# Optimization experiments

Measured on AMD Instinct MI355X. Metric: run time of the kernel, lower is better.

## Reference

```python
import jax, jax.numpy as jnp
import numpy as np

N_EMBD = 1024
N_HEAD = 16
HEAD_DIM = N_EMBD // N_HEAD


def setup_inputs() -> dict:
    key = jax.random.key(0)
    ks = jax.random.split(key, 9)
    B, T, C = 2, 2048, N_EMBD
    s = 1.0 / np.sqrt(C)
    inp = {
        "x": jax.random.normal(ks[0], (B, T, C), dtype=jnp.float32),
        "Wq": jax.random.normal(ks[1], (C, C), dtype=jnp.float32) * s,
        "bq": jnp.zeros((C,), dtype=jnp.float32),
        "Wk": jax.random.normal(ks[2], (C, C), dtype=jnp.float32) * s,
        "bk": jnp.zeros((C,), dtype=jnp.float32),
        "Wv": jax.random.normal(ks[3], (C, C), dtype=jnp.float32) * s,
        "bv": jnp.zeros((C,), dtype=jnp.float32),
        "Wo": jax.random.normal(ks[4], (C, C), dtype=jnp.float32) * s,
        "bo": jnp.zeros((C,), dtype=jnp.float32),
    }
    return inp


def reference(x, Wq, bq, Wk, bk, Wv, bv, Wo, bo):
    B, T, C = x.shape
    H, D = N_HEAD, HEAD_DIM
    # projections (torch Linear: x @ W^T + b)
    q = (x @ Wq.T + bq).reshape(B, T, H, D).transpose(0, 2, 1, 3)  # [B,H,T,D]
    k = (x @ Wk.T + bk).reshape(B, T, H, D).transpose(0, 2, 1, 3)
    v = (x @ Wv.T + bv).reshape(B, T, H, D).transpose(0, 2, 1, 3)
    scores = jnp.einsum("bhqd,bhkd->bhqk", q, k) / jnp.sqrt(jnp.asarray(D, x.dtype))
    causal = jnp.tril(jnp.ones((T, T), dtype=bool))
    scores = jnp.where(causal[None, None], scores, jnp.asarray(-jnp.inf, x.dtype))
    weights = jax.nn.softmax(scores, axis=-1)  # [B,H,T,T]
    attended = jnp.einsum("bhqk,bhkd->bhqd", weights, v)
    attended = attended.transpose(0, 2, 1, 3).reshape(B, T, C)
    return attended @ Wo.T + bo
```

## Files before the change

kernel.cpp:

```cpp
#include <hip/hip_runtime.h>

typedef unsigned short u16;
typedef __attribute__((ext_vector_type(8))) __bf16 bf16x8;
typedef __attribute__((ext_vector_type(4))) float f32x4;
typedef __attribute__((ext_vector_type(4))) unsigned int u32x4;

#define MFMA16(a, b, c) __builtin_amdgcn_mfma_f32_16x16x32_bf16(a, b, c, 0, 0, 0)

__device__ __forceinline__ u16 f2bf(float f) {
    unsigned u = __float_as_uint(f);
    u = (u + 0x7FFFu + ((u >> 16) & 1u)) >> 16;
    return (u16)u;
}

__device__ __forceinline__ void gl_lds16(const u16* g, u16* l) {
    __builtin_amdgcn_global_load_lds(
        (const __attribute__((address_space(1))) unsigned int*)g,
        (__attribute__((address_space(3))) unsigned int*)l, 16, 0, 0);
}

static constexpr int Bv = 2, Tv = 2048, Cv = 1024, Hv = 16, Dv = 64;
static constexpr int Mv = Bv * Tv;

static constexpr size_t OFF_XB = 0;
static constexpr size_t OFF_WQ = 4194304;
static constexpr size_t OFF_WK = OFF_WQ + 1048576;
static constexpr size_t OFF_WV = OFF_WK + 1048576;
static constexpr size_t OFF_WO = OFF_WV + 1048576;
static constexpr size_t OFF_Q  = OFF_WO + 1048576;
static constexpr size_t OFF_K  = OFF_Q + 4194304;
static constexpr size_t OFF_VT = OFF_K + 4194304;
static constexpr size_t OFF_A  = OFF_VT + 4194304;

__global__ __launch_bounds__(256) void convert_all(
    const float* __restrict__ x,
    const float* __restrict__ wq, const float* __restrict__ wk,
    const float* __restrict__ wv, const float* __restrict__ wo,
    u16* __restrict__ dst)
{
    int i4 = blockIdx.x * blockDim.x + threadIdx.x;
    if (i4 >= 2097152) return;
    int idx = i4 * 4;
    const float* src; int off;
    if (idx < 4194304) { src = x; off = idx; }
    else {
        int rel = idx - 4194304;
        int j = rel >> 20;
        off = rel & 1048575;
        src = (j == 0) ? wq : (j == 1) ? wk : (j == 2) ? wv : wo;
    }
    float4 v = *(const float4*)(src + off);
    ushort4 o;
    o.x = f2bf(v.x); o.y = f2bf(v.y); o.z = f2bf(v.z); o.w = f2bf(v.w);
    *(ushort4*)(dst + idx) = o;
}

template <bool OUT_BF16, bool ROWBIAS>
__device__ __forceinline__ void gemm128_b32(
    u16* __restrict__ lA0, u16* __restrict__ lB0,
    u16* __restrict__ lA1, u16* __restrict__ lB1,
    const u16* __restrict__ A, const u16* __restrict__ Wt,
    const float* __restrict__ bias, void* __restrict__ outp,
    int m0, int n0, int N, int K)
{
    const int tid  = threadIdx.x;
    const int lane = tid & 63, w = tid >> 6;
    const int quad = lane >> 4, lm = lane & 15;
    const int wm = (w & 1) * 64, wn = (w >> 1) * 64;
    const int h4A = (w & 1) * 4, h4B = ((w >> 1) & 1) * 4;
    const int rowi = lane >> 3, seg = lane & 7;
    const int raw = seg ^ rowi;
    const int hh  = raw >> 2, qq = raw & 3;

    f32x4 zero = {0.f, 0.f, 0.f, 0.f};
    f32x4 acc[4][4];
    #pragma unroll
    for (int mt = 0; mt < 4; mt++)
        #pragma unroll
        for (int nt = 0; nt < 4; nt++) acc[mt][nt] = zero;

    auto stage = [&](u16* dA, u16* dB, int k0) __attribute__((always_inline)) {
        #pragma unroll
        for (int j = 0; j < 2; j++) {
            int pr0 = w * 16 + j * 8;
            int gr  = pr0 + rowi + (hh << 6);
            gl_lds16(A  + (size_t)(m0 + gr) * K + k0 + qq * 8, &dA[pr0 * 64]);
            gl_lds16(Wt + (size_t)(n0 + gr) * K + k0 + qq * 8, &dB[pr0 * 64]);
        }
    };
    auto compute = [&](const u16* sA, const u16* sB) __attribute__((always_inline)) {
        bf16x8 af[4], bf[4];
        #pragma unroll
        for (int mt = 0; mt < 4; mt++)
            af[mt] = *(const bf16x8*)&sA[(mt * 16 + lm) * 64 + (((h4A + quad) ^ (lm & 7)) * 8)];
        #pragma unroll
        for (int nt = 0; nt < 4; nt++)
            bf[nt] = *(const bf16x8*)&sB[(nt * 16 + lm) * 64 + (((h4B + quad) ^ (lm & 7)) * 8)];
        #pragma unroll
        for (int mt = 0; mt < 4; mt++)
            #pragma unroll
            for (int nt = 0; nt < 4; nt++)
                acc[mt][nt] = MFMA16(af[mt], bf[nt], acc[mt][nt]);
    };

    const int NT = K >> 5;
    stage(lA0, lB0, 0);
    stage(lA1, lB1, 32);
    for (int t = 0; t < NT; ++t) {
        if (t + 1 < NT) asm volatile("s_waitcnt vmcnt(4)" ::: "memory");
        else            asm volatile("s_waitcnt vmcnt(0)" ::: "memory");
        __builtin_amdgcn_s_barrier();
        const u16* sA = (t & 1) ? lA1 : lA0;
        const u16* sB = (t & 1) ? lB1 : lB0;
        compute(sA, sB);
        asm volatile("s_waitcnt lgkmcnt(0)" ::: "memory");
        __builtin_amdgcn_s_barrier();
        if (t + 2 < NT) stage((t & 1) ? lA1 : lA0, (t & 1) ? lB1 : lB0, (t + 2) << 5);
    }

    #pragma unroll
    for (int nt = 0; nt < 4; nt++) {
        int col = n0 + wn + nt * 16 + lm;
        float cb = ROWBIAS ? 0.f : bias[col];
        #pragma unroll
        for (int mt = 0; mt < 4; mt++) {
            #pragma unroll
            for (int r = 0; r < 4; r++) {
                int row = m0 + wm + mt * 16 + quad * 4 + r;
                float v = acc[mt][nt][r] + (ROWBIAS ? bias[row] : cb);
                if (OUT_BF16) ((u16*)outp)[(size_t)row * N + col] = f2bf(v);
                else          ((float*)outp)[(size_t)row * N + col] = v;
            }
        }
    }
}

__global__ __launch_bounds__(256, 3) void gemm_qkv(
    const u16* __restrict__ A,
    const u16* __restrict__ Wq, const u16* __restrict__ Wk, const u16* __restrict__ Wv,
    const float* __restrict__ bq, const float* __restrict__ bk, const float* __restrict__ bv,
    u16* __restrict__ Q, u16* __restrict__ K, u16* __restrict__ VT)
{
    __shared__ u16 lA0[64 * 64];
    __shared__ u16 lB0[64 * 64];
    __shared__ u16 lA1[64 * 64];
    __shared__ u16 lB1[64 * 64];

    int bid = blockIdx.x;
    int sw  = (bid & 7) * 96 + (bid >> 3);
    int g2  = sw >> 5;
    int row = sw & 31;
    int which = g2 >> 3, col = g2 & 7;

    if (which == 0) {
        gemm128_b32<true, false>(lA0, lB0, lA1, lB1, A, Wq, bq, Q, row * 128, col * 128, Cv, Cv);
    } else if (which == 1) {
        gemm128_b32<true, false>(lA0, lB0, lA1, lB1, A, Wk, bk, K, row * 128, col * 128, Cv, Cv);
    } else {
        gemm128_b32<true, true>(lA0, lB0, lA1, lB1, Wv, A, bv, VT, col * 128, row * 128, Mv, Cv);
    }
}

__global__ __launch_bounds__(512) void gemm_o64(
    const u16* __restrict__ A, const u16* __restrict__ Wt,
    const float* __restrict__ bias, float* __restrict__ outp)
{
    __shared__ u16 lA0[128 * 64];
    __shared__ u16 lA1[128 * 64];
    __shared__ u16 lB0[64 * 64];
    __shared__ u16 lB1[64 * 64];

    const int tid  = threadIdx.x;
    const int lane = tid & 63, w = tid >> 6;
    const int quad = lane >> 4, lm = lane & 15;
    const int wm = (w & 3) * 32, wn = (w >> 2) * 32;

    int bid = blockIdx.x;
    int sw  = (bid & 7) * 64 + (bid >> 3);
    const int n0 = (sw >> 5) * 64;
    const int m0 = (sw & 31) * 128;
    const int K = Cv;
    const int rowi = lane >> 3, seg = lane & 7;

    f32x4 zero = {0.f, 0.f, 0.f, 0.f};
    f32x4 acc[2][2];
    #pragma unroll
    for (int mt = 0; mt < 2; mt++)
        #pragma unroll
        for (int nt = 0; nt < 2; nt++) acc[mt][nt] = zero;

    auto stage = [&](u16* dA, u16* dB, int k0) __attribute__((always_inline)) {
        #pragma unroll
        for (int i = 0; i < 2; i++) {
            int rbase = w * 16 + i * 8;
            int row = rbase + rowi;
            int gseg = seg ^ (row & 7);
            gl_lds16(A + (size_t)(m0 + row) * K + k0 + gseg * 8, &dA[rbase * 64]);
        }
        {
            int rbase = w * 8, row = rbase + rowi;
            gl_lds16(Wt + (size_t)(n0 + row) * K + k0 + ((seg ^ (row & 7))) * 8, &dB[rbase * 64]);
        }
    };
    auto compute = [&](const u16* sA, const u16* sB) __attribute__((always_inline)) {
        #pragma unroll
        for (int ks = 0; ks < 2; ks++) {
            const int swz = ((ks * 4 + quad) ^ (lm & 7)) * 8;
            bf16x8 af[2], bf[2];
            #pragma unroll
            for (int mt = 0; mt < 2; mt++)
                af[mt] = *(const bf16x8*)&sA[(wm + mt * 16 + lm) * 64 + swz];
            #pragma unroll
            for (int nt = 0; nt < 2; nt++)
                bf[nt] = *(const bf16x8*)&sB[(wn + nt * 16 + lm) * 64 + swz];
            #pragma unroll
            for (int mt = 0; mt < 2; mt++)
                #pragma unroll
                for (int nt = 0; nt < 2; nt++)
                    acc[mt][nt] = MFMA16(af[mt], bf[nt], acc[mt][nt]);
        }
    };

    const int NT = K >> 6;
    stage(lA0, lB0, 0);
    stage(lA1, lB1, 64);
    for (int t = 0; t < NT; ++t) {
        if (t + 1 < NT) asm volatile("s_waitcnt vmcnt(3)" ::: "memory");
        else            asm volatile("s_waitcnt vmcnt(0)" ::: "memory");
        __builtin_amdgcn_s_barrier();
        u16* sA = (t & 1) ? lA1 : lA0;
        u16* sB = (t & 1) ? lB1 : lB0;
        compute(sA, sB);
        asm volatile("s_waitcnt lgkmcnt(0)" ::: "memory");
        __builtin_amdgcn_s_barrier();
        if (t + 2 < NT) stage(sA, sB, (t + 2) << 6);
    }

    #pragma unroll
    for (int nt = 0; nt < 2; nt++) {
        int col = n0 + wn + nt * 16 + lm;
        float bvv = bias[col];
        #pragma unroll
        for (int mt = 0; mt < 2; mt++) {
            #pragma unroll
            for (int r = 0; r < 4; r++) {
                int row = m0 + wm + mt * 16 + quad * 4 + r;
                outp[(size_t)row * Cv + col] = acc[mt][nt][r] + bvv;
            }
        }
    }
}

__global__ __launch_bounds__(512) void attn(
    const u16* __restrict__ Qp, const u16* __restrict__ Kp,
    const u16* __restrict__ VTg, u16* __restrict__ Op)
{
    __shared__ u16 lK[2][64 * 64];
    __shared__ u16 lVT[2][64 * 64];
    __shared__ u16 lP[8][32][72];

    const int tid  = threadIdx.x;
    const int lane = tid & 63, w = tid >> 6;
    const int g = w >> 2, wl = w & 3;
    const int quad = lane >> 4, lm = lane & 15;

    const int idx  = blockIdx.x;
    const int half = idx >> 8;
    const int grp  = idx & 255;
    const int bh   = (half << 4) | (grp >> 4);
    const int j    = grp & 15;
    const int qt   = half ? j : 15 - j;
    const int h = bh & 15, b = bh >> 4;

    const int qb = qt * 128;
    const size_t headoff = (size_t)b * Tv * Cv + (size_t)h * Dv;
    const size_t vthead  = (size_t)h * 64 * Mv + (size_t)b * Tv;

    bf16x8 qf[2][2];
    #pragma unroll
    for (int nt = 0; nt < 2; nt++) {
        const u16* qptr = Qp + headoff + (size_t)(qb + wl * 32 + nt * 16 + lm) * Cv + quad * 8;
        qf[0][nt] = *(const bf16x8*)(qptr);
        qf[1][nt] = *(const bf16x8*)(qptr + 32);
    }

    f32x4 zero = {0.f, 0.f, 0.f, 0.f};
    f32x4 oacc[2][4];
    #pragma unroll
    for (int mt = 0; mt < 2; mt++)
        #pragma unroll
        for (int nt = 0; nt < 4; nt++) oacc[mt][nt] = zero;
    float Lp[2] = {0.f, 0.f};

    const float SC = 0.18033688011112042f;
    const int rowi = lane >> 3, seg = lane & 7;

    auto stage = [&](int kt) {
        const int k0 = kt * 64;
        #pragma unroll
        for (int hf = 0; hf < 2; hf++) {
            int rbase = wl * 16 + hf * 8;
            int row = rbase + rowi;
            int gseg = seg ^ (row & 7);
            gl_lds16(Kp + headoff + (size_t)(k0 + row) * Cv + gseg * 8, &lK[g][rbase * 64]);
            gl_lds16(VTg + vthead + (size_t)row * Mv + k0 + gseg * 8, &lVT[g][rbase * 64]);
        }
    };

    auto body = [&](int kt, bool domask) __attribute__((always_inline)) {
        const int k0 = kt * 64;
        f32x4 stt[4][2];
        #pragma unroll
        for (int mt = 0; mt < 4; mt++)
            #pragma unroll
            for (int nt = 0; nt < 2; nt++) stt[mt][nt] = zero;
        #pragma unroll
        for (int ks = 0; ks < 2; ks++) {
            #pragma unroll
            for (int mt = 0; mt < 4; mt++) {
                bf16x8 kf = *(const bf16x8*)
                    &lK[g][(mt * 16 + lm) * 64 + (((ks * 4 + quad) ^ (lm & 7)) * 8)];
                #pragma unroll
                for (int nt = 0; nt < 2; nt++)
                    stt[mt][nt] = MFMA16(kf, qf[ks][nt], stt[mt][nt]);
            }
        }
        #pragma unroll
        for (int mt = 0; mt < 4; mt++) {
            #pragma unroll
            for (int nt = 0; nt < 2; nt++) {
                const int keyb = k0 + mt * 16 + quad * 4;
                const int qrow = qb + wl * 32 + nt * 16 + lm;
                float e0 = __builtin_amdgcn_exp2f(fmaf(stt[mt][nt][0], SC, -16.f));
                float e1 = __builtin_amdgcn_exp2f(fmaf(stt[mt][nt][1], SC, -16.f));
                float e2 = __builtin_amdgcn_exp2f(fmaf(stt[mt][nt][2], SC, -16.f));
                float e3 = __builtin_amdgcn_exp2f(fmaf(stt[mt][nt][3], SC, -16.f));
                if (domask) {
                    if (keyb + 0 > qrow) e0 = 0.f;
                    if (keyb + 1 > qrow) e1 = 0.f;
                    if (keyb + 2 > qrow) e2 = 0.f;
                    if (keyb + 3 > qrow) e3 = 0.f;
                }
                Lp[nt] += e0 + e1 + e2 + e3;
                ushort4 pk;
                pk.x = (u16)(__float_as_uint(e0) >> 16);
                pk.y = (u16)(__float_as_uint(e1) >> 16);
                pk.z = (u16)(__float_as_uint(e2) >> 16);
                pk.w = (u16)(__float_as_uint(e3) >> 16);
                *(ushort4*)&lP[w][nt * 16 + lm][mt * 16 + quad * 4] = pk;
            }
        }
        #pragma unroll
        for (int ks = 0; ks < 2; ks++) {
            bf16x8 pf[2];
            #pragma unroll
            for (int mt = 0; mt < 2; mt++)
                pf[mt] = *(const bf16x8*)&lP[w][mt * 16 + lm][ks * 32 + quad * 8];
            #pragma unroll
            for (int nt = 0; nt < 4; nt++) {
                bf16x8 vf = *(const bf16x8*)
                    &lVT[g][(nt * 16 + lm) * 64 + (((ks * 4 + quad) ^ (lm & 7)) * 8)];
                #pragma unroll
                for (int mt = 0; mt < 2; mt++)
                    oacc[mt][nt] = MFMA16(pf[mt], vf, oacc[mt][nt]);
            }
        }
    };

    for (int i = 0; i < qt; i++) {
        if (i) __syncthreads();
        stage(2 * i + g);
        __syncthreads();
        body(2 * i + g, false);
    }
    if (qt) __syncthreads();
    stage(2 * qt + g);
    __syncthreads();
    body(2 * qt + g, true);
    __syncthreads();

    float* lO = (float*)&lP[0][0][0];
    float* lL = lO + 32 * 256;
    const int t = tid & 255;
    if (g == 1) {
        #pragma unroll
        for (int mt = 0; mt < 2; mt++)
            #pragma unroll
            for (int nt = 0; nt < 4; nt++)
                #pragma unroll
                for (int r = 0; r < 4; r++)
                    lO[(mt * 16 + nt * 4 + r) * 256 + t] = oacc[mt][nt][r];
        lL[t] = Lp[0];
        lL[256 + t] = Lp[1];
    }
    __syncthreads();
    if (g == 0) {
        #pragma unroll
        for (int mt = 0; mt < 2; mt++)
            #pragma unroll
            for (int nt = 0; nt < 4; nt++)
                #pragma unroll
                for (int r = 0; r < 4; r++)
                    oacc[mt][nt][r] += lO[(mt * 16 + nt * 4 + r) * 256 + t];
        Lp[0] += lL[t];
        Lp[1] += lL[256 + t];

        float Lred[2];
        #pragma unroll
        for (int nt = 0; nt < 2; nt++) {
            float L = Lp[nt];
            L += __shfl_xor(L, 16, 64);
            L += __shfl_xor(L, 32, 64);
            Lred[nt] = 1.0f / L;
        }
        #pragma unroll
        for (int mt = 0; mt < 2; mt++) {
            float inv[4];
            #pragma unroll
            for (int r = 0; r < 4; r++)
                inv[r] = __shfl(Lred[mt], (lane & 48) | (quad * 4 + r), 64);
            #pragma unroll
            for (int nt = 0; nt < 4; nt++) {
                #pragma unroll
                for (int r = 0; r < 4; r++) {
                    int row = qb + wl * 32 + mt * 16 + quad * 4 + r;
                    Op[headoff + (size_t)row * Cv + nt * 16 + lm] = f2bf(oacc[mt][nt][r] * inv[r]);
                }
            }
        }
    }
}

extern "C" void kernel_launch(void* const* d_in, const int* in_sizes, int n_in,
                              void* d_out, int out_size, void* d_ws, size_t ws_size,
                              hipStream_t stream) {
    const float* x  = (const float*)d_in[0];
    const float* Wq = (const float*)d_in[1];
    const float* bq = (const float*)d_in[2];
    const float* Wk = (const float*)d_in[3];
    const float* bk = (const float*)d_in[4];
    const float* Wv = (const float*)d_in[5];
    const float* bv = (const float*)d_in[6];
    const float* Wo = (const float*)d_in[7];
    const float* bo = (const float*)d_in[8];
    u16* ws = (u16*)d_ws;

    convert_all<<<8192, 256, 0, stream>>>(x, Wq, Wk, Wv, Wo, ws);

    gemm_qkv<<<768, 256, 0, stream>>>(
        ws + OFF_XB, ws + OFF_WQ, ws + OFF_WK, ws + OFF_WV,
        bq, bk, bv, ws + OFF_Q, ws + OFF_K, ws + OFF_VT);

    attn<<<512, 512, 0, stream>>>(ws + OFF_Q, ws + OFF_K, ws + OFF_VT, ws + OFF_A);

    gemm_o64<<<512, 512, 0, stream>>>(ws + OFF_A, ws + OFF_WO, bo, (float*)d_out);
}
```

Measured before the change: 177.1 us.

## Reuse shared 128x128 GEMM for output projection and raise MFMA priority in attention

The output projection kernel drops its custom 128x64 tile, 512-thread implementation and calls the shared gemm128_b32 routine with 128x128 tiles, 256 threads and 256 blocks. The aim is more data reuse per block and fewer launched blocks. Separately, the attention kernel wraps its two MFMA phases in s_setprio(1)/s_setprio(0) so matrix work gets scheduling priority over the exp/softmax phase of other waves. The trade-off is that the larger tiles give only 256 blocks, which may leave some compute units underused.

```diff
diff --git a/kernel.cpp b/kernel.cpp
--- a/kernel.cpp
+++ b/kernel.cpp
@@ -161,94 +161,22 @@
     }
 }
 
-__global__ __launch_bounds__(512) void gemm_o64(
+__global__ __launch_bounds__(256, 3) void gemm_o64(
     const u16* __restrict__ A, const u16* __restrict__ Wt,
     const float* __restrict__ bias, float* __restrict__ outp)
 {
-    __shared__ u16 lA0[128 * 64];
-    __shared__ u16 lA1[128 * 64];
+    __shared__ u16 lA0[64 * 64];
     __shared__ u16 lB0[64 * 64];
+    __shared__ u16 lA1[64 * 64];
     __shared__ u16 lB1[64 * 64];
 
-    const int tid  = threadIdx.x;
-    const int lane = tid & 63, w = tid >> 6;
-    const int quad = lane >> 4, lm = lane & 15;
-    const int wm = (w & 3) * 32, wn = (w >> 2) * 32;
-
     int bid = blockIdx.x;
-    int sw  = (bid & 7) * 64 + (bid >> 3);
-    const int n0 = (sw >> 5) * 64;
-    const int m0 = (sw & 31) * 128;
-    const int K = Cv;
-    const int rowi = lane >> 3, seg = lane & 7;
-
-    f32x4 zero = {0.f, 0.f, 0.f, 0.f};
-    f32x4 acc[2][2];
-    #pragma unroll
-    for (int mt = 0; mt < 2; mt++)
-        #pragma unroll
-        for (int nt = 0; nt < 2; nt++) acc[mt][nt] = zero;
-
-    auto stage = [&](u16* dA, u16* dB, int k0) __attribute__((always_inline)) {
-        #pragma unroll
-        for (int i = 0; i < 2; i++) {
-            int rbase = w * 16 + i * 8;
-            int row = rbase + rowi;
-            int gseg = seg ^ (row & 7);
-            gl_lds16(A + (size_t)(m0 + row) * K + k0 + gseg * 8, &dA[rbase * 64]);
-        }
-        {
-            int rbase = w * 8, row = rbase + rowi;
-            gl_lds16(Wt + (size_t)(n0 + row) * K + k0 + ((seg ^ (row & 7))) * 8, &dB[rbase * 64]);
-        }
-    };
-    auto compute = [&](const u16* sA, const u16* sB) __attribute__((always_inline)) {
-        #pragma unroll
-        for (int ks = 0; ks < 2; ks++) {
-            const int swz = ((ks * 4 + quad) ^ (lm & 7)) * 8;
-            bf16x8 af[2], bf[2];
-            #pragma unroll
-            for (int mt = 0; mt < 2; mt++)
-                af[mt] = *(const bf16x8*)&sA[(wm + mt * 16 + lm) * 64 + swz];
-            #pragma unroll
-            for (int nt = 0; nt < 2; nt++)
-                bf[nt] = *(const bf16x8*)&sB[(wn + nt * 16 + lm) * 64 + swz];
-            #pragma unroll
-            for (int mt = 0; mt < 2; mt++)
-                #pragma unroll
-                for (int nt = 0; nt < 2; nt++)
-                    acc[mt][nt] = MFMA16(af[mt], bf[nt], acc[mt][nt]);
-        }
-    };
-
-    const int NT = K >> 6;
-    stage(lA0, lB0, 0);
-    stage(lA1, lB1, 64);
-    for (int t = 0; t < NT; ++t) {
-        if (t + 1 < NT) asm volatile("s_waitcnt vmcnt(3)" ::: "memory");
-        else            asm volatile("s_waitcnt vmcnt(0)" ::: "memory");
-        __builtin_amdgcn_s_barrier();
-        u16* sA = (t & 1) ? lA1 : lA0;
-        u16* sB = (t & 1) ? lB1 : lB0;
-        compute(sA, sB);
-        asm volatile("s_waitcnt lgkmcnt(0)" ::: "memory");
-        __builtin_amdgcn_s_barrier();
-        if (t + 2 < NT) stage(sA, sB, (t + 2) << 6);
-    }
-
-    #pragma unroll
-    for (int nt = 0; nt < 2; nt++) {
-        int col = n0 + wn + nt * 16 + lm;
-        float bvv = bias[col];
-        #pragma unroll
-        for (int mt = 0; mt < 2; mt++) {
-            #pragma unroll
-            for (int r = 0; r < 4; r++) {
-                int row = m0 + wm + mt * 16 + quad * 4 + r;
-                outp[(size_t)row * Cv + col] = acc[mt][nt][r] + bvv;
-            }
-        }
-    }
+    int sw  = (bid & 7) * 32 + (bid >> 3);
+    int col = sw >> 5;
+    int row = sw & 31;
+
+    gemm128_b32<false, false>(lA0, lB0, lA1, lB1, A, Wt, bias, outp,
+                              row * 128, col * 128, Cv, Cv);
 }
 
 __global__ __launch_bounds__(512) void attn(
@@ -314,6 +242,7 @@
         for (int mt = 0; mt < 4; mt++)
             #pragma unroll
             for (int nt = 0; nt < 2; nt++) stt[mt][nt] = zero;
+        __builtin_amdgcn_s_setprio(1);
         #pragma unroll
         for (int ks = 0; ks < 2; ks++) {
             #pragma unroll
@@ -325,6 +254,7 @@
                     stt[mt][nt] = MFMA16(kf, qf[ks][nt], stt[mt][nt]);
             }
         }
+        __builtin_amdgcn_s_setprio(0);
         #pragma unroll
         for (int mt = 0; mt < 4; mt++) {
             #pragma unroll
@@ -350,6 +280,7 @@
                 *(ushort4*)&lP[w][nt * 16 + lm][mt * 16 + quad * 4] = pk;
             }
         }
+        __builtin_amdgcn_s_setprio(1);
         #pragma unroll
         for (int ks = 0; ks < 2; ks++) {
             bf16x8 pf[2];
@@ -365,6 +296,7 @@
                     oacc[mt][nt] = MFMA16(pf[mt], vf, oacc[mt][nt]);
             }
         }
+        __builtin_amdgcn_s_setprio(0);
     };
 
     for (int i = 0; i < qt; i++) {
@@ -453,5 +385,5 @@
 
     attn<<<512, 512, 0, stream>>>(ws + OFF_Q, ws + OFF_K, ws + OFF_VT, ws + OFF_A);
 
-    gemm_o64<<<512, 512, 0, stream>>>(ws + OFF_A, ws + OFF_WO, bo, (float*)d_out);
-}
+    gemm_o64<<<256, 256, 0, stream>>>(ws + OFF_A, ws + OFF_WO, bo, (float*)d_out);
+}
```

Measured after the change: 175.7 us. No clear change (-0.8%).
